# Kernel tuning notes

Measured on AMD Instinct MI355X. Metric: run time of the kernel, lower is better.

## Reference

```python
import jax, jax.numpy as jnp
import numpy as np

D_MODEL = 1024
NUM_HEADS = 16
D_K = D_MODEL // NUM_HEADS


def setup_inputs() -> dict:
    key = jax.random.key(0)
    ks = jax.random.split(key, 12)
    B, L, D = 1, 4096, D_MODEL
    s = 1.0 / np.sqrt(D)
    return {
        "q": jax.random.normal(ks[0], (B, L, D), jnp.float32),
        "k": jax.random.normal(ks[1], (B, L, D), jnp.float32),
        "v": jax.random.normal(ks[2], (B, L, D), jnp.float32),
        "wq": jax.random.normal(ks[3], (D, D), jnp.float32) * s,
        "bq": jnp.zeros((D,), jnp.float32),
        "wk": jax.random.normal(ks[4], (D, D), jnp.float32) * s,
        "bk": jnp.zeros((D,), jnp.float32),
        "wv": jax.random.normal(ks[5], (D, D), jnp.float32) * s,
        "bv": jnp.zeros((D,), jnp.float32),
        "wo": jax.random.normal(ks[6], (D, D), jnp.float32) * s,
        "bo": jnp.zeros((D,), jnp.float32),
    }


def reference(q, k, v, wq, bq, wk, bk, wv, bv, wo, bo):
    B, L, D = q.shape
    H, dk = NUM_HEADS, D_K
    # linear projections then split heads: [B, L, D] -> [B, H, L, dk]
    def proj(x, w, b):
        return (x @ w.T + b).reshape(B, L, H, dk).transpose(0, 2, 1, 3)
    qh = proj(q, wq, bq)
    kh = proj(k, wk, bk)
    vh = proj(v, wv, bv)
    scores = jnp.einsum("bhqd,bhkd->bhqk", qh, kh) / jnp.sqrt(jnp.float32(dk))
    attn = jax.nn.softmax(scores, axis=-1)  # [B, H, L, L]
    out = jnp.einsum("bhqk,bhkd->bhqd", attn, vh)
    out = out.transpose(0, 2, 1, 3).reshape(B, L, D)
    return out @ wo.T + bo
```

## Files before the change

### kernel.cpp

```cpp
#include <hip/hip_runtime.h>
#include <hip/hip_bf16.h>
#include <stdint.h>


typedef __bf16 bf16_t;
typedef __bf16 bf16x8 __attribute__((ext_vector_type(8)));
typedef __bf16 bf16x4 __attribute__((ext_vector_type(4)));
typedef float f32x4 __attribute__((ext_vector_type(4)));

#define MFMA_BF16 __builtin_amdgcn_mfma_f32_16x16x32_bf16

__device__ __forceinline__ void async_copy16(const void* g, void* lds) {
  __builtin_amdgcn_global_load_lds(
      (__attribute__((address_space(1))) void*)(uintptr_t)g,
      (__attribute__((address_space(3))) void*)lds, 16, 0, 0);
}

__global__ __launch_bounds__(256) void cast_f32_bf16(
    const float* __restrict__ s0, bf16_t* __restrict__ d0, int n0,
    const float* __restrict__ s1, bf16_t* __restrict__ d1, int n1,
    const float* __restrict__ s2, bf16_t* __restrict__ d2, int n2,
    const float* __restrict__ s3, bf16_t* __restrict__ d3, int n3,
    const float* __restrict__ s4, bf16_t* __restrict__ d4, int n4,
    const float* __restrict__ s5, bf16_t* __restrict__ d5, int n5,
    const float* __restrict__ s6, bf16_t* __restrict__ d6, int n6) {
  const float* s;
  bf16_t* d;
  int n;
  switch (blockIdx.z) {
    case 0: s = s0; d = d0; n = n0; break;
    case 1: s = s1; d = d1; n = n1; break;
    case 2: s = s2; d = d2; n = n2; break;
    case 3: s = s3; d = d3; n = n3; break;
    case 4: s = s4; d = d4; n = n4; break;
    case 5: s = s5; d = d5; n = n5; break;
    default: s = s6; d = d6; n = n6; break;
  }
  const int i = (blockIdx.x * 256 + threadIdx.x) * 8;
  if (i >= n) return;
  float4 a = *(const float4*)(s + i);
  float4 b = *(const float4*)(s + i + 4);
  bf16x8 o;
  o[0] = (bf16_t)a.x; o[1] = (bf16_t)a.y; o[2] = (bf16_t)a.z; o[3] = (bf16_t)a.w;
  o[4] = (bf16_t)b.x; o[5] = (bf16_t)b.y; o[6] = (bf16_t)b.z; o[7] = (bf16_t)b.w;
  *(bf16x8*)(d + i) = o;
}

__global__ __launch_bounds__(256) void gemm_qkv(
    const bf16_t* __restrict__ A0, const bf16_t* __restrict__ W0,
    const float* __restrict__ b0,
    const bf16_t* __restrict__ A1, const bf16_t* __restrict__ W1,
    const float* __restrict__ b1,
    const bf16_t* __restrict__ A2, const bf16_t* __restrict__ W2,
    const float* __restrict__ b2,
    bf16_t* __restrict__ Qt, bf16_t* __restrict__ Kt,
    bf16_t* __restrict__ Vt, int M, int N, int K) {
  const bf16_t *A, *W;
  const float* bias;
  bf16_t* C;
  const int z = blockIdx.z;
  if (z == 0)      { A = A0; W = W0; bias = b0; C = Qt; }
  else if (z == 1) { A = A1; W = W1; bias = b1; C = Kt; }
  else             { A = A2; W = W2; bias = b2; C = Vt; }

  __shared__ bf16_t As[128][32];
  __shared__ bf16_t Bs[128][32];

  const int t = threadIdx.x;
  const int w = t >> 6, lane = t & 63;
  const int quad = lane >> 4, l16 = lane & 15;
  const int wr = w >> 1, wc = w & 1;
  const int m0 = blockIdx.x * 128;
  const int n0 = blockIdx.y * 128;
  const int srow = lane >> 2;
  const int scol = (lane & 3) * 8;

  f32x4 acc[4][4] = {};

  for (int k0 = 0; k0 < K; k0 += 32) {
    async_copy16(&A[(size_t)(m0 + (2 * w) * 16 + srow) * K + k0 + scol],
                 (char*)As + (2 * w) * 1024);
    async_copy16(&A[(size_t)(m0 + (2 * w + 1) * 16 + srow) * K + k0 + scol],
                 (char*)As + (2 * w + 1) * 1024);
    async_copy16(&W[(size_t)(n0 + (2 * w) * 16 + srow) * K + k0 + scol],
                 (char*)Bs + (2 * w) * 1024);
    async_copy16(&W[(size_t)(n0 + (2 * w + 1) * 16 + srow) * K + k0 + scol],
                 (char*)Bs + (2 * w + 1) * 1024);
    __syncthreads();

    bf16x8 af[4], bfr[4];
#pragma unroll
    for (int mt = 0; mt < 4; mt++)
      af[mt] = *(const bf16x8*)&As[wr * 64 + mt * 16 + l16][quad * 8];
#pragma unroll
    for (int nt = 0; nt < 4; nt++)
      bfr[nt] = *(const bf16x8*)&Bs[wc * 64 + nt * 16 + l16][quad * 8];
#pragma unroll
    for (int mt = 0; mt < 4; mt++)
#pragma unroll
      for (int nt = 0; nt < 4; nt++)
        acc[mt][nt] = MFMA_BF16(af[mt], bfr[nt], acc[mt][nt], 0, 0, 0);
    __syncthreads();
  }

  if (z < 2) {
    const float scale = (z == 0) ? 0.125f * 1.44269504088896340736f : 1.0f;
#pragma unroll
    for (int nt = 0; nt < 4; nt++) {
      const int col = n0 + wc * 64 + nt * 16 + l16;
      const float bb = bias[col];
      const size_t base_nt = (size_t)(col >> 6) * 262144 +
                             ((col >> 5) & 1) * 512 + ((col >> 3) & 3) * 128 +
                             (col & 7);
#pragma unroll
      for (int mt = 0; mt < 4; mt++) {
        const int tile = (m0 >> 4) + wr * 4 + mt;
        const size_t tb = base_nt + (size_t)tile * 1024;
#pragma unroll
        for (int r = 0; r < 4; r++)
          C[tb + (quad * 4 + r) * 8] = (bf16_t)((acc[mt][nt][r] + bb) * scale);
      }
    }
  } else {
#pragma unroll
    for (int nt = 0; nt < 4; nt++) {
      const int col = n0 + wc * 64 + nt * 16 + l16;
      const int dk = col & 63;
      const float bb = bias[col];
      const size_t hb = (size_t)(col >> 6) * 262144 +
                        (size_t)(dk >> 4) * 1024 + (dk & 15) * 8;
#pragma unroll
      for (int mt = 0; mt < 4; mt++) {
        const int rb = m0 + wr * 64 + mt * 16 + quad * 4;
        const size_t addr = hb + (size_t)(rb >> 6) * 4096 +
                            ((rb >> 5) & 1) * 512 + ((rb >> 3) & 3) * 128 +
                            (rb & 7);
        bf16x4 pk;
#pragma unroll
        for (int r = 0; r < 4; r++) pk[r] = (bf16_t)(acc[mt][nt][r] + bb);
        *(bf16x4*)&C[addr] = pk;
      }
    }
  }
}

__global__ __launch_bounds__(256) void gemm_out(
    const bf16_t* __restrict__ A, const bf16_t* __restrict__ W,
    const float* __restrict__ bias, float* __restrict__ C, int M, int N,
    int K) {
  __shared__ bf16_t As[128][32];
  __shared__ bf16_t Bs[128][32];

  const int t = threadIdx.x;
  const int w = t >> 6, lane = t & 63;
  const int quad = lane >> 4, l16 = lane & 15;
  const int wr = w >> 1, wc = w & 1;
  const int m0 = blockIdx.x * 128;
  const int n0 = blockIdx.y * 128;
  const int srow = lane >> 2;
  const int scol = (lane & 3) * 8;

  f32x4 acc[4][4] = {};

  for (int k0 = 0; k0 < K; k0 += 32) {
    async_copy16(&A[(size_t)(m0 + (2 * w) * 16 + srow) * K + k0 + scol],
                 (char*)As + (2 * w) * 1024);
    async_copy16(&A[(size_t)(m0 + (2 * w + 1) * 16 + srow) * K + k0 + scol],
                 (char*)As + (2 * w + 1) * 1024);
    async_copy16(&W[(size_t)(n0 + (2 * w) * 16 + srow) * K + k0 + scol],
                 (char*)Bs + (2 * w) * 1024);
    async_copy16(&W[(size_t)(n0 + (2 * w + 1) * 16 + srow) * K + k0 + scol],
                 (char*)Bs + (2 * w + 1) * 1024);
    __syncthreads();

    bf16x8 af[4], bfr[4];
#pragma unroll
    for (int mt = 0; mt < 4; mt++)
      af[mt] = *(const bf16x8*)&As[wr * 64 + mt * 16 + l16][quad * 8];
#pragma unroll
    for (int nt = 0; nt < 4; nt++)
      bfr[nt] = *(const bf16x8*)&Bs[wc * 64 + nt * 16 + l16][quad * 8];
#pragma unroll
    for (int mt = 0; mt < 4; mt++)
#pragma unroll
      for (int nt = 0; nt < 4; nt++)
        acc[mt][nt] = MFMA_BF16(af[mt], bfr[nt], acc[mt][nt], 0, 0, 0);
    __syncthreads();
  }

#pragma unroll
  for (int nt = 0; nt < 4; nt++) {
    const int col = n0 + wc * 64 + nt * 16 + l16;
    const float bb = bias[col];
#pragma unroll
    for (int mt = 0; mt < 4; mt++) {
#pragma unroll
      for (int r = 0; r < 4; r++) {
        const int row = m0 + wr * 64 + mt * 16 + quad * 4 + r;
        C[(size_t)row * N + col] = acc[mt][nt][r] + bb;
      }
    }
  }
}

__global__ __launch_bounds__(256, 2) void flash_attn(
    const bf16_t* __restrict__ Qt, const bf16_t* __restrict__ Kt,
    const bf16_t* __restrict__ Vt, bf16_t* __restrict__ O, int L) {
  const int h = blockIdx.y;
  const int t = threadIdx.x;
  const int w = t >> 6, lane = t & 63;
  const int quad = lane >> 4, l16 = lane & 15;
  const int tq0 = blockIdx.x * 8 + w * 2;

  __shared__ bf16_t Kst[2][4096];
  __shared__ bf16_t Pb[4][32][72];

  const size_t hb = (size_t)h * 262144;

  bf16x8 qa[2][2];
#pragma unroll
  for (int qt = 0; qt < 2; qt++)
#pragma unroll
    for (int kc = 0; kc < 2; kc++)
      qa[qt][kc] = *(const bf16x8*)(Qt + hb + (size_t)(tq0 + qt) * 1024 +
                                    kc * 512 + lane * 8);

#define STAGE(it_, buf_)                                                     \
  {                                                                          \
    const size_t cb = hb + (size_t)(it_) * 4096;                             \
    async_copy16(Kt + cb + (size_t)t * 8, (char*)&Kst[buf_][0] + w * 1024);  \
    async_copy16(Kt + cb + (size_t)(256 + t) * 8,                            \
                 (char*)&Kst[buf_][0] + 4096 + w * 1024);                    \
  }

  STAGE(0, 0);

  f32x4 oT[2][4] = {};
  float ls[2] = {0.f, 0.f};

  const int NIT = L / 64;
  for (int it = 0; it < NIT; it++) {
    const int buf = it & 1;
    __syncthreads();
    if (it + 1 < NIT) STAGE(it + 1, buf ^ 1);

    bf16x8 vb[4][2];
#pragma unroll
    for (int dkt = 0; dkt < 4; dkt++)
#pragma unroll
      for (int kvc = 0; kvc < 2; kvc++)
        vb[dkt][kvc] = *(const bf16x8*)(Vt + hb + (size_t)(it * 4 + dkt) * 1024 +
                                        kvc * 512 + lane * 8);

    bf16x8 kb[4][2];
#pragma unroll
    for (int tt = 0; tt < 4; tt++)
#pragma unroll
      for (int kc = 0; kc < 2; kc++)
        kb[tt][kc] = *(const bf16x8*)((const char*)&Kst[buf][0] + tt * 2048 +
                                      kc * 1024 + lane * 16);

#pragma unroll
    for (int qt = 0; qt < 2; qt++) {
      f32x4 sT[4];
#pragma unroll
      for (int tt = 0; tt < 4; tt++) {
        f32x4 z = {0.f, 0.f, 0.f, 0.f};
        z = MFMA_BF16(kb[tt][0], qa[qt][0], z, 0, 0, 0);
        z = MFMA_BF16(kb[tt][1], qa[qt][1], z, 0, 0, 0);
        sT[tt] = z;
      }
#pragma unroll
      for (int tt = 0; tt < 4; tt++) {
        bf16x4 pk;
        float rs = 0.f;
#pragma unroll
        for (int r = 0; r < 4; r++) {
          const float p = __builtin_amdgcn_exp2f(sT[tt][r]);
          rs += p;
          pk[r] = (bf16_t)p;
        }
        ls[qt] += rs;
        *(bf16x4*)&Pb[w][qt * 16 + l16][tt * 16 + quad * 4] = pk;
      }
    }

#pragma unroll
    for (int qt = 0; qt < 2; qt++) {
      const bf16x8 pf0 = *(const bf16x8*)&Pb[w][qt * 16 + l16][quad * 8];
      const bf16x8 pf1 = *(const bf16x8*)&Pb[w][qt * 16 + l16][32 + quad * 8];
#pragma unroll
      for (int dkt = 0; dkt < 4; dkt++) {
        oT[qt][dkt] = MFMA_BF16(vb[dkt][0], pf0, oT[qt][dkt], 0, 0, 0);
        oT[qt][dkt] = MFMA_BF16(vb[dkt][1], pf1, oT[qt][dkt], 0, 0, 0);
      }
    }
  }
#undef STAGE

#pragma unroll
  for (int qt = 0; qt < 2; qt++) {
    float l = ls[qt];
    l += __shfl_xor(l, 16);
    l += __shfl_xor(l, 32);
    const float inv = 1.0f / l;
    const size_t row = (size_t)(tq0 + qt) * 16 + l16;
#pragma unroll
    for (int dkt = 0; dkt < 4; dkt++)
#pragma unroll
      for (int r = 0; r < 4; r++)
        O[row * 1024 + h * 64 + dkt * 16 + quad * 4 + r] =
            (bf16_t)(oT[qt][dkt][r] * inv);
  }
}

extern "C" void kernel_launch(void* const* d_in, const int* in_sizes, int n_in,
                              void* d_out, int out_size, void* d_ws,
                              size_t ws_size, hipStream_t stream) {
  const float* q  = (const float*)d_in[0];
  const float* k  = (const float*)d_in[1];
  const float* v  = (const float*)d_in[2];
  const float* wq = (const float*)d_in[3];
  const float* bq = (const float*)d_in[4];
  const float* wk = (const float*)d_in[5];
  const float* bk = (const float*)d_in[6];
  const float* wv = (const float*)d_in[7];
  const float* bv = (const float*)d_in[8];
  const float* wo = (const float*)d_in[9];
  const float* bo = (const float*)d_in[10];
  float* out = (float*)d_out;

  const int L = 4096, D = 1024;
  const int nLD = L * D;
  const int nDD = D * D;
  bf16_t* p = (bf16_t*)d_ws;
  bf16_t* qb  = p; p += nLD;
  bf16_t* kb  = p; p += nLD;
  bf16_t* vb  = p; p += nLD;
  bf16_t* wqb = p; p += nDD;
  bf16_t* wkb = p; p += nDD;
  bf16_t* wvb = p; p += nDD;
  bf16_t* wob = p; p += nDD;
  bf16_t* Qt  = p; p += nLD;
  bf16_t* Kt  = p; p += nLD;
  bf16_t* Vt  = p; p += nLD;
  bf16_t* Op  = qb;

  dim3 blk(256);
  cast_f32_bf16<<<dim3(nLD / (256 * 8), 1, 7), blk, 0, stream>>>(
      q, qb, nLD, k, kb, nLD, v, vb, nLD, wq, wqb, nDD, wk, wkb, nDD,
      wv, wvb, nDD, wo, wob, nDD);
  gemm_qkv<<<dim3(L / 128, D / 128, 3), blk, 0, stream>>>(
      qb, wqb, bq, kb, wkb, bk, vb, wvb, bv, Qt, Kt, Vt, L, D, D);
  flash_attn<<<dim3(L / 128, 16), blk, 0, stream>>>(Qt, Kt, Vt, Op, L);
  gemm_out<<<dim3(L / 128, D / 128), blk, 0, stream>>>(Op, wob, bo, out, L, D,
                                                       D);
}
```

Before: 275.3 us.

## Fuse fp32-to-bf16 casts into GEMM loads and shrink output GEMM tile

Removes the separate cast kernel and has the QKV and output GEMMs read fp32 inputs and weights directly, converting to bf16 as they store into shared memory. This drops a full extra pass over the inputs and weights through bf16 workspace buffers. The output GEMM also moves to 64-row tiles to launch more blocks. In exchange, loads become synchronous register round-trips instead of async global-to-LDS copies, and fp32 reads double bytes per tile, while weights are reconverted by every block.

```diff
diff --git a/kernel.cpp b/kernel.cpp
--- a/kernel.cpp
+++ b/kernel.cpp
@@ -16,47 +16,23 @@
       (__attribute__((address_space(3))) void*)lds, 16, 0, 0);
 }
 
-__global__ __launch_bounds__(256) void cast_f32_bf16(
-    const float* __restrict__ s0, bf16_t* __restrict__ d0, int n0,
-    const float* __restrict__ s1, bf16_t* __restrict__ d1, int n1,
-    const float* __restrict__ s2, bf16_t* __restrict__ d2, int n2,
-    const float* __restrict__ s3, bf16_t* __restrict__ d3, int n3,
-    const float* __restrict__ s4, bf16_t* __restrict__ d4, int n4,
-    const float* __restrict__ s5, bf16_t* __restrict__ d5, int n5,
-    const float* __restrict__ s6, bf16_t* __restrict__ d6, int n6) {
-  const float* s;
-  bf16_t* d;
-  int n;
-  switch (blockIdx.z) {
-    case 0: s = s0; d = d0; n = n0; break;
-    case 1: s = s1; d = d1; n = n1; break;
-    case 2: s = s2; d = d2; n = n2; break;
-    case 3: s = s3; d = d3; n = n3; break;
-    case 4: s = s4; d = d4; n = n4; break;
-    case 5: s = s5; d = d5; n = n5; break;
-    default: s = s6; d = d6; n = n6; break;
-  }
-  const int i = (blockIdx.x * 256 + threadIdx.x) * 8;
-  if (i >= n) return;
-  float4 a = *(const float4*)(s + i);
-  float4 b = *(const float4*)(s + i + 4);
-  bf16x8 o;
-  o[0] = (bf16_t)a.x; o[1] = (bf16_t)a.y; o[2] = (bf16_t)a.z; o[3] = (bf16_t)a.w;
-  o[4] = (bf16_t)b.x; o[5] = (bf16_t)b.y; o[6] = (bf16_t)b.z; o[7] = (bf16_t)b.w;
-  *(bf16x8*)(d + i) = o;
-}
-
-__global__ __launch_bounds__(256) void gemm_qkv(
-    const bf16_t* __restrict__ A0, const bf16_t* __restrict__ W0,
+__device__ __forceinline__ bf16x4 cvt4(float4 v) {
+  bf16x4 o;
+  o[0] = (bf16_t)v.x; o[1] = (bf16_t)v.y;
+  o[2] = (bf16_t)v.z; o[3] = (bf16_t)v.w;
+  return o;
+}
+
+__global__ __launch_bounds__(256) void gemm_qkv_f32(
+    const float* __restrict__ A0, const float* __restrict__ W0,
     const float* __restrict__ b0,
-    const bf16_t* __restrict__ A1, const bf16_t* __restrict__ W1,
+    const float* __restrict__ A1, const float* __restrict__ W1,
     const float* __restrict__ b1,
-    const bf16_t* __restrict__ A2, const bf16_t* __restrict__ W2,
+    const float* __restrict__ A2, const float* __restrict__ W2,
     const float* __restrict__ b2,
     bf16_t* __restrict__ Qt, bf16_t* __restrict__ Kt,
     bf16_t* __restrict__ Vt, int M, int N, int K) {
-  const bf16_t *A, *W;
-  const float* bias;
+  const float *A, *W, *bias;
   bf16_t* C;
   const int z = blockIdx.z;
   if (z == 0)      { A = A0; W = W0; bias = b0; C = Qt; }
@@ -72,20 +48,20 @@
   const int wr = w >> 1, wc = w & 1;
   const int m0 = blockIdx.x * 128;
   const int n0 = blockIdx.y * 128;
-  const int srow = lane >> 2;
-  const int scol = (lane & 3) * 8;
+  const int srow = t >> 3;
+  const int scol = (t & 7) * 4;
 
   f32x4 acc[4][4] = {};
 
   for (int k0 = 0; k0 < K; k0 += 32) {
-    async_copy16(&A[(size_t)(m0 + (2 * w) * 16 + srow) * K + k0 + scol],
-                 (char*)As + (2 * w) * 1024);
-    async_copy16(&A[(size_t)(m0 + (2 * w + 1) * 16 + srow) * K + k0 + scol],
-                 (char*)As + (2 * w + 1) * 1024);
-    async_copy16(&W[(size_t)(n0 + (2 * w) * 16 + srow) * K + k0 + scol],
-                 (char*)Bs + (2 * w) * 1024);
-    async_copy16(&W[(size_t)(n0 + (2 * w + 1) * 16 + srow) * K + k0 + scol],
-                 (char*)Bs + (2 * w + 1) * 1024);
+#pragma unroll
+    for (int p = 0; p < 4; p++) {
+      const int r = p * 32 + srow;
+      float4 av = *(const float4*)&A[(size_t)(m0 + r) * K + k0 + scol];
+      float4 wv = *(const float4*)&W[(size_t)(n0 + r) * K + k0 + scol];
+      *(bf16x4*)&As[r][scol] = cvt4(av);
+      *(bf16x4*)&Bs[r][scol] = cvt4(wv);
+    }
     __syncthreads();
 
     bf16x8 af[4], bfr[4];
@@ -145,43 +121,45 @@
 }
 
 __global__ __launch_bounds__(256) void gemm_out(
-    const bf16_t* __restrict__ A, const bf16_t* __restrict__ W,
+    const bf16_t* __restrict__ A, const float* __restrict__ W,
     const float* __restrict__ bias, float* __restrict__ C, int M, int N,
     int K) {
-  __shared__ bf16_t As[128][32];
+  __shared__ bf16_t As[64][32];
   __shared__ bf16_t Bs[128][32];
 
   const int t = threadIdx.x;
   const int w = t >> 6, lane = t & 63;
   const int quad = lane >> 4, l16 = lane & 15;
   const int wr = w >> 1, wc = w & 1;
-  const int m0 = blockIdx.x * 128;
+  const int m0 = blockIdx.x * 64;
   const int n0 = blockIdx.y * 128;
-  const int srow = lane >> 2;
-  const int scol = (lane & 3) * 8;
-
-  f32x4 acc[4][4] = {};
+  const int arow = lane >> 2;
+  const int acol = (lane & 3) * 8;
+  const int srow = t >> 3;
+  const int scol = (t & 7) * 4;
+
+  f32x4 acc[2][4] = {};
 
   for (int k0 = 0; k0 < K; k0 += 32) {
-    async_copy16(&A[(size_t)(m0 + (2 * w) * 16 + srow) * K + k0 + scol],
-                 (char*)As + (2 * w) * 1024);
-    async_copy16(&A[(size_t)(m0 + (2 * w + 1) * 16 + srow) * K + k0 + scol],
-                 (char*)As + (2 * w + 1) * 1024);
-    async_copy16(&W[(size_t)(n0 + (2 * w) * 16 + srow) * K + k0 + scol],
-                 (char*)Bs + (2 * w) * 1024);
-    async_copy16(&W[(size_t)(n0 + (2 * w + 1) * 16 + srow) * K + k0 + scol],
-                 (char*)Bs + (2 * w + 1) * 1024);
-    __syncthreads();
-
-    bf16x8 af[4], bfr[4];
-#pragma unroll
-    for (int mt = 0; mt < 4; mt++)
-      af[mt] = *(const bf16x8*)&As[wr * 64 + mt * 16 + l16][quad * 8];
+    async_copy16(&A[(size_t)(m0 + w * 16 + arow) * K + k0 + acol],
+                 (char*)As + w * 1024);
+#pragma unroll
+    for (int p = 0; p < 4; p++) {
+      const int r = p * 32 + srow;
+      float4 wv = *(const float4*)&W[(size_t)(n0 + r) * K + k0 + scol];
+      *(bf16x4*)&Bs[r][scol] = cvt4(wv);
+    }
+    __syncthreads();
+
+    bf16x8 af[2], bfr[4];
+#pragma unroll
+    for (int mt = 0; mt < 2; mt++)
+      af[mt] = *(const bf16x8*)&As[wr * 32 + mt * 16 + l16][quad * 8];
 #pragma unroll
     for (int nt = 0; nt < 4; nt++)
       bfr[nt] = *(const bf16x8*)&Bs[wc * 64 + nt * 16 + l16][quad * 8];
 #pragma unroll
-    for (int mt = 0; mt < 4; mt++)
+    for (int mt = 0; mt < 2; mt++)
 #pragma unroll
       for (int nt = 0; nt < 4; nt++)
         acc[mt][nt] = MFMA_BF16(af[mt], bfr[nt], acc[mt][nt], 0, 0, 0);
@@ -193,10 +171,10 @@
     const int col = n0 + wc * 64 + nt * 16 + l16;
     const float bb = bias[col];
 #pragma unroll
-    for (int mt = 0; mt < 4; mt++) {
+    for (int mt = 0; mt < 2; mt++) {
 #pragma unroll
       for (int r = 0; r < 4; r++) {
-        const int row = m0 + wr * 64 + mt * 16 + quad * 4 + r;
+        const int row = m0 + wr * 32 + mt * 16 + quad * 4 + r;
         C[(size_t)row * N + col] = acc[mt][nt][r] + bb;
       }
     }
@@ -249,7 +227,8 @@
     for (int dkt = 0; dkt < 4; dkt++)
 #pragma unroll
       for (int kvc = 0; kvc < 2; kvc++)
-        vb[dkt][kvc] = *(const bf16x8*)(Vt + hb + (size_t)(it * 4 + dkt) * 1024 +
+        vb[dkt][kvc] = *(const bf16x8*)(Vt + hb +
+                                        (size_t)(it * 4 + dkt) * 1024 +
                                         kvc * 512 + lane * 8);
 
     bf16x8 kb[4][2];
@@ -332,27 +311,16 @@
 
   const int L = 4096, D = 1024;
   const int nLD = L * D;
-  const int nDD = D * D;
   bf16_t* p = (bf16_t*)d_ws;
-  bf16_t* qb  = p; p += nLD;
-  bf16_t* kb  = p; p += nLD;
-  bf16_t* vb  = p; p += nLD;
-  bf16_t* wqb = p; p += nDD;
-  bf16_t* wkb = p; p += nDD;
-  bf16_t* wvb = p; p += nDD;
-  bf16_t* wob = p; p += nDD;
-  bf16_t* Qt  = p; p += nLD;
-  bf16_t* Kt  = p; p += nLD;
-  bf16_t* Vt  = p; p += nLD;
-  bf16_t* Op  = qb;
+  bf16_t* Qt = p; p += nLD;
+  bf16_t* Kt = p; p += nLD;
+  bf16_t* Vt = p; p += nLD;
+  bf16_t* Op = p; p += nLD;
 
   dim3 blk(256);
-  cast_f32_bf16<<<dim3(nLD / (256 * 8), 1, 7), blk, 0, stream>>>(
-      q, qb, nLD, k, kb, nLD, v, vb, nLD, wq, wqb, nDD, wk, wkb, nDD,
-      wv, wvb, nDD, wo, wob, nDD);
-  gemm_qkv<<<dim3(L / 128, D / 128, 3), blk, 0, stream>>>(
-      qb, wqb, bq, kb, wkb, bk, vb, wvb, bv, Qt, Kt, Vt, L, D, D);
+  gemm_qkv_f32<<<dim3(L / 128, D / 128, 3), blk, 0, stream>>>(
+      q, wq, bq, k, wk, bk, v, wv, bv, Qt, Kt, Vt, L, D, D);
   flash_attn<<<dim3(L / 128, 16), blk, 0, stream>>>(Qt, Kt, Vt, Op, L);
-  gemm_out<<<dim3(L / 128, D / 128), blk, 0, stream>>>(Op, wob, bo, out, L, D,
-                                                       D);
-}
+  gemm_out<<<dim3(L / 64, D / 128), blk, 0, stream>>>(Op, wo, bo, out, L, D,
+                                                      D);
+}
```

Measured after the change: 284.9 us. +3.5%, slower.
